# Kernel optimization log

Measured on AMD Instinct MI355X. Metric: run time of the kernel, lower is better.

## Reference

```python
import jax, jax.numpy as jnp
import numpy as np

H, D, DM, L, B = 16, 64, 1024, 256, 64
SCALE = 1.0 / np.sqrt(D)   # 1/sqrt(d_head)
CHUNK = 64
LN_EPS = 1e-5


def setup_inputs() -> dict:
    key = jax.random.key(0)
    k0, k1, k2, k3 = jax.random.split(key, 4)
    h = jax.random.normal(k0, (L, B, DM), jnp.float32)
    qkv_w = jax.random.normal(k1, (H * 4 * D, DM), jnp.float32) * 0.02
    o_w = jax.random.normal(k2, (DM, H * D), jnp.float32) * 0.02
    ln_gamma = jnp.ones((DM,), jnp.float32)
    ln_beta = jnp.zeros((DM,), jnp.float32)
    pi0 = jax.random.uniform(k3, (H, 256), jnp.float32)
    return {"h": h, "qkv_w": qkv_w, "o_w": o_w,
            "ln_gamma": ln_gamma, "ln_beta": ln_beta, "pi0": pi0}


def _phi(x):
    # elu(x) + 1, then sum-normalize over feature dim
    e = jax.nn.elu(x) + 1.0
    return e / e.sum(-1, keepdims=True)


def _fast_weight_sum(q, k, v):
    # q,k,v: [B,H,L,D]. out[t] = q_t @ W_t, W_t = sum_{s<=t} k_s v_s^T (inclusive).
    # Chunked-recurrent form: intra-chunk causal GEMM + inter-chunk carried state.
    Bb, Hh, Ll, Dd = q.shape
    nc = Ll // CHUNK
    rs = lambda x: x.reshape(Bb, Hh, nc, CHUNK, Dd).transpose(2, 0, 1, 3, 4)  # [nc,B,H,C,D]
    qc, kc, vc = rs(q), rs(k), rs(v)
    mask = jnp.tril(jnp.ones((CHUNK, CHUNK), q.dtype))  # inclusive causal

    def step(W, xs):
        qi, ki, vi = xs  # [B,H,C,D]
        scores = jnp.einsum('bhtd,bhsd->bhts', qi, ki) * mask
        out = jnp.einsum('bhts,bhsd->bhtd', scores, vi) \
            + jnp.einsum('bhtd,bhde->bhte', qi, W)
        W = W + jnp.einsum('bhsd,bhse->bhde', ki, vi)
        return W, out

    W0 = jnp.zeros((Bb, Hh, Dd, Dd), q.dtype)
    _, outs = jax.lax.scan(step, W0, (qc, kc, vc))  # outs: [nc,B,H,C,D]
    return outs.transpose(1, 2, 0, 3, 4).reshape(Bb, Hh, Ll, Dd)


def reference(h, qkv_w, o_w, ln_gamma, ln_beta, pi0):
    slen, bsz, _ = h.shape
    # qkv projection and head split (rbf2keys: q, k1, k2, v)
    qkv = (h @ qkv_w.T).reshape(slen, bsz, H, 4 * D)
    hq, hk1, hk2, hv = jnp.split(qkv, 4, axis=-1)       # each [L,B,H,D]
    perm = lambda x: x.transpose(1, 2, 0, 3)            # -> [B,H,L,D]
    hq, hk1, hk2, hv = perm(hq), perm(hk1), perm(hk2), perm(hv)

    hq = _phi(hq)
    hk1 = _phi(hk1)
    hk2 = _phi(hk2)

    out1 = _fast_weight_sum(hq, hk1, hv)
    out2 = _fast_weight_sum(hq, hk2, hv)

    # skip_attn_normalization=True path: pi0-gated mixture of the two memories
    p = jnp.clip(pi0, 0.0, 1.0)[None, :, :slen, None]   # [1,H,L,1]
    layer_out = SCALE * (out1 * p + out2 * (1.0 - p))   # [B,H,L,D]

    # [B,H,L,D] -> [L,B,H*D]
    layer_out = layer_out.transpose(0, 2, 1, 3).reshape(bsz, slen, H * D).transpose(1, 0, 2)
    attn_out = layer_out @ o_w.T                        # [L,B,DM]

    # post-LN residual (pre_lnorm=False)
    x = h + attn_out
    mu = x.mean(-1, keepdims=True)
    var = ((x - mu) ** 2).mean(-1, keepdims=True)
    return (x - mu) / jnp.sqrt(var + LN_EPS) * ln_gamma + ln_beta
```

## Files before the change

### kernel.cpp

```cpp
#include <hip/hip_runtime.h>
#include <type_traits>


typedef short v8s __attribute__((ext_vector_type(8)));
typedef float v4f __attribute__((ext_vector_type(4)));

__device__ __forceinline__ float bf2f(short s) {
    unsigned int u = ((unsigned int)(unsigned short)s) << 16;
    float f;
    __builtin_memcpy(&f, &u, 4);
    return f;
}
__device__ __forceinline__ short f2bf(float f) {
    unsigned int u;
    __builtin_memcpy(&u, &f, 4);
    u = u + 0x7fffu + ((u >> 16) & 1u);
    return (short)(u >> 16);
}

__device__ __forceinline__ void load_lds16(const short* g, short* l) {
    __builtin_amdgcn_global_load_lds((const __attribute__((address_space(1))) void*)g,
                                     (__attribute__((address_space(3))) void*)l, 16, 0, 0);
}

__global__ void __launch_bounds__(256)
cvt_bf16(const float* __restrict__ in, short* __restrict__ out, int n4) {
    int i = blockIdx.x * 256 + threadIdx.x;
    if (i >= n4) return;
    float4 v = ((const float4*)in)[i];
    short4 o;
    o.x = f2bf(v.x); o.y = f2bf(v.y); o.z = f2bf(v.z); o.w = f2bf(v.w);
    ((short4*)out)[i] = o;
}

template <typename OutT>
__global__ void __launch_bounds__(512, 2)
gemm_nt(const short* __restrict__ Ap, const short* __restrict__ Bp,
        OutT* __restrict__ C, int M, int N, int K) {
    __shared__ __align__(16) short lds[2][2][256 * 64];

    const int tid = threadIdx.x;
    const int w = tid >> 6, lane = tid & 63;
    const int wm = w >> 2, wn = w & 3;
    const int lq = lane >> 4, lr = lane & 15;
    const int asw = (lr & 7) * 8;
    const int rr = tid >> 3;
    const int scol = ((tid & 7) * 8) ^ ((rr & 7) * 8);

    int bid = blockIdx.y * gridDim.x + blockIdx.x;
    int nwg = gridDim.x * gridDim.y;
    int swz = (bid & 7) * (nwg >> 3) + (bid >> 3);
    int bm = swz % gridDim.x, bn = swz / gridDim.x;

    v4f acc[8][4] = {};
    v8s a[4][2];
    v8s b[2][2][2];

    const int NT = K >> 6;
    const int nIter = NT >> 1;

#define BAR_() do { asm volatile("" ::: "memory"); __builtin_amdgcn_s_barrier(); asm volatile("" ::: "memory"); } while (0)
#define SBAR_() __builtin_amdgcn_sched_barrier(0)
#define VMCNT4_() asm volatile("s_waitcnt vmcnt(4)" ::: "memory")
#define STAGE_(MAT, BUF, HALF, KT) do { \
        const short* g_ = ((MAT) ? Bp : Ap) + \
            (long)(((MAT) ? bn : bm) * 256 + (HALF) * 128 + rr) * K + (KT) * 64 + scol; \
        short* l_ = &lds[BUF][MAT][(HALF) * 8192] + w * 512; \
        load_lds16(g_, l_); \
        load_lds16(g_ + (long)64 * K, l_ + 4096); \
    } while (0)
#define LDA_(QM, BUF) do { \
        _Pragma("unroll") \
        for (int mi = 0; mi < 4; ++mi) { \
            const short* pa_ = &lds[BUF][0][(wm * 128 + (QM) * 64 + mi * 16 + lr) * 64]; \
            a[mi][0] = *(const v8s*)&pa_[(lq * 8) ^ asw]; \
            a[mi][1] = *(const v8s*)&pa_[(32 + lq * 8) ^ asw]; \
        } \
    } while (0)
#define LDB_(QN, BUF) do { \
        _Pragma("unroll") \
        for (int ni = 0; ni < 2; ++ni) { \
            const short* pb_ = &lds[BUF][1][(wn * 64 + (QN) * 32 + ni * 16 + lr) * 64]; \
            b[QN][ni][0] = *(const v8s*)&pb_[(lq * 8) ^ asw]; \
            b[QN][ni][1] = *(const v8s*)&pb_[(32 + lq * 8) ^ asw]; \
        } \
    } while (0)
#define MFMA_(QM, QN) do { \
        __builtin_amdgcn_s_setprio(1); \
        _Pragma("unroll") \
        for (int kk = 0; kk < 2; ++kk) \
            _Pragma("unroll") \
            for (int mi = 0; mi < 4; ++mi) \
                _Pragma("unroll") \
                for (int ni = 0; ni < 2; ++ni) \
                    acc[(QM) * 4 + mi][(QN) * 2 + ni] = __builtin_amdgcn_mfma_f32_16x16x32_bf16( \
                        a[mi][kk], b[QN][ni][kk], acc[(QM) * 4 + mi][(QN) * 2 + ni], 0, 0, 0); \
        __builtin_amdgcn_s_setprio(0); \
    } while (0)

    STAGE_(1, 0, 0, 0);
    STAGE_(1, 0, 1, 0);
    STAGE_(0, 0, 0, 0);
    STAGE_(0, 0, 1, 0);
    STAGE_(1, 1, 0, 1);
    STAGE_(1, 1, 1, 1);
    VMCNT4_();
    BAR_();

    for (int it = 0; it < nIter; ++it) {
        const int t1 = 2 * it + 1;
        int t2 = 2 * it + 2; if (t2 >= NT) t2 -= NT;
        int t3 = 2 * it + 3; if (t3 >= NT) t3 -= NT;

        LDA_(0, 0); LDB_(0, 0); LDB_(1, 0);
        STAGE_(0, 1, 0, t1);
        MFMA_(0, 0);
        SBAR_(); BAR_();
        STAGE_(0, 1, 1, t1);
        MFMA_(0, 1);
        SBAR_();
        LDA_(1, 0);
        SBAR_(); BAR_();
        STAGE_(1, 0, 0, t2);
        MFMA_(1, 0);
        SBAR_(); BAR_();
        STAGE_(1, 0, 1, t2);
        VMCNT4_();
        MFMA_(1, 1);
        SBAR_(); BAR_();
        LDA_(0, 1); LDB_(0, 1); LDB_(1, 1);
        STAGE_(0, 0, 0, t2);
        MFMA_(0, 0);
        SBAR_(); BAR_();
        STAGE_(0, 0, 1, t2);
        MFMA_(0, 1);
        SBAR_();
        LDA_(1, 1);
        SBAR_(); BAR_();
        STAGE_(1, 1, 0, t3);
        MFMA_(1, 0);
        SBAR_(); BAR_();
        STAGE_(1, 1, 1, t3);
        VMCNT4_();
        MFMA_(1, 1);
        SBAR_(); BAR_();
    }

#undef BAR_
#undef SBAR_
#undef VMCNT4_
#undef STAGE_
#undef LDA_
#undef LDB_
#undef MFMA_

#pragma unroll
    for (int m = 0; m < 8; ++m)
#pragma unroll
        for (int n = 0; n < 4; ++n)
#pragma unroll
            for (int r = 0; r < 4; ++r) {
                int row = bm * 256 + wm * 128 + m * 16 + lq * 4 + r;
                int col = bn * 256 + wn * 64 + n * 16 + lr;
                float v = acc[m][n][r];
                if constexpr (std::is_same_v<OutT, short>)
                    C[(long)row * N + col] = f2bf(v);
                else
                    C[(long)row * N + col] = v;
            }
}

#define SW(row, s) ((row) * 72 + ((((s) >> 3) ^ (((row) >> 4) & 7)) << 3) + ((s) & 7))

__device__ __forceinline__ void phi_store(const short* __restrict__ g,
                                          short* sS, short* sT, int r, int seg) {
    union { int4 v[2]; short s[16]; } u;
    u.v[0] = *(const int4*)(g);
    u.v[1] = *(const int4*)(g + 8);
    float f[16]; float ssum = 0.f;
#pragma unroll
    for (int i = 0; i < 16; i++) {
        float x = bf2f(u.s[i]);
        float e = x > 0.f ? x + 1.f : __expf(x);
        f[i] = e; ssum += e;
    }
    ssum += __shfl_xor(ssum, 1, 64);
    ssum += __shfl_xor(ssum, 2, 64);
    float inv = 1.f / ssum;
    union { int4 v[2]; short s[16]; } o;
#pragma unroll
    for (int i = 0; i < 16; i++) o.s[i] = f2bf(f[i] * inv);
    *(int4*)&sS[SW(r, seg)] = o.v[0];
    *(int4*)&sS[SW(r, seg + 8)] = o.v[1];
    if (sT) {
#pragma unroll
        for (int i = 0; i < 16; i++) sT[SW(seg + i, r)] = o.s[i];
    }
}

__global__ void __launch_bounds__(256)
fastweight(const short* __restrict__ qkv, const float* __restrict__ pi0,
           short* __restrict__ outm) {
    const int bid = blockIdx.x;
    const int h = bid & 15, b = bid >> 4;
    const int tid = threadIdx.x;
    const int w = tid >> 6, lane = tid & 63;
    const int lq = lane >> 4, lr = lane & 15;
    __shared__ __align__(16) short sq[64 * 72];
    __shared__ __align__(16) short sk1S[64 * 72];
    __shared__ __align__(16) short sk2S[64 * 72];
    __shared__ __align__(16) short sk1T[64 * 72];
    __shared__ __align__(16) short sk2T[64 * 72];
    __shared__ __align__(16) short svT[64 * 72];
    __shared__ __align__(16) short sW1T[64 * 72];
    __shared__ __align__(16) short sW2T[64 * 72];
    __shared__ float spi[256];

    for (int i = tid; i < 64 * 36; i += 256) { ((int*)sW1T)[i] = 0; ((int*)sW2T)[i] = 0; }
    spi[tid] = pi0[h * 256 + tid];

    const int r = tid >> 2, seg = (tid & 3) * 16;

    v4f wacc1[4] = {}, wacc2[4] = {};

    for (int c = 0; c < 4; c++) {
        __syncthreads();
        const long gbase = ((long)((c * 64 + r) * 64 + b)) * 4096 + h * 256;
        phi_store(qkv + gbase + seg, sq, nullptr, r, seg);
        phi_store(qkv + gbase + 64 + seg, sk1S, sk1T, r, seg);
        phi_store(qkv + gbase + 128 + seg, sk2S, sk2T, r, seg);
        {
            union { int4 v[2]; short s[16]; } u;
            u.v[0] = *(const int4*)(qkv + gbase + 192 + seg);
            u.v[1] = *(const int4*)(qkv + gbase + 192 + seg + 8);
#pragma unroll
            for (int i = 0; i < 16; i++) svT[SW(seg + i, r)] = u.s[i];
        }
        __syncthreads();

        v8s qa0 = *(const v8s*)&sq[SW(16 * w + lr, lq * 8)];
        v8s qa1 = *(const v8s*)&sq[SW(16 * w + lr, 32 + lq * 8)];

        v4f sacc1[4], sacc2[4];
#pragma unroll
        for (int n = 0; n < 4; n++) {
            v8s b10 = *(const v8s*)&sk1S[SW(16 * n + lr, lq * 8)];
            v8s b11 = *(const v8s*)&sk1S[SW(16 * n + lr, 32 + lq * 8)];
            v8s b20 = *(const v8s*)&sk2S[SW(16 * n + lr, lq * 8)];
            v8s b21 = *(const v8s*)&sk2S[SW(16 * n + lr, 32 + lq * 8)];
            v4f t1 = {}, t2 = {};
            t1 = __builtin_amdgcn_mfma_f32_16x16x32_bf16(qa0, b10, t1, 0, 0, 0);
            t2 = __builtin_amdgcn_mfma_f32_16x16x32_bf16(qa0, b20, t2, 0, 0, 0);
            t1 = __builtin_amdgcn_mfma_f32_16x16x32_bf16(qa1, b11, t1, 0, 0, 0);
            t2 = __builtin_amdgcn_mfma_f32_16x16x32_bf16(qa1, b21, t2, 0, 0, 0);
            sacc1[n] = t1; sacc2[n] = t2;
        }
        __syncthreads();
#pragma unroll
        for (int n = 0; n < 4; n++)
#pragma unroll
            for (int rr = 0; rr < 4; rr++) {
                int t_ = 16 * w + lq * 4 + rr;
                int s_ = 16 * n + lr;
                sk1S[SW(t_, s_)] = f2bf(s_ <= t_ ? sacc1[n][rr] : 0.f);
                sk2S[SW(t_, s_)] = f2bf(s_ <= t_ ? sacc2[n][rr] : 0.f);
            }

        v8s sa10 = *(const v8s*)&sk1S[SW(16 * w + lr, lq * 8)];
        v8s sa11 = *(const v8s*)&sk1S[SW(16 * w + lr, 32 + lq * 8)];
        v8s sa20 = *(const v8s*)&sk2S[SW(16 * w + lr, lq * 8)];
        v8s sa21 = *(const v8s*)&sk2S[SW(16 * w + lr, 32 + lq * 8)];
        v4f o1[4], o2[4];
#pragma unroll
        for (int n = 0; n < 4; n++) {
            v8s vb0 = *(const v8s*)&svT[SW(16 * n + lr, lq * 8)];
            v8s vb1 = *(const v8s*)&svT[SW(16 * n + lr, 32 + lq * 8)];
            v8s wb10 = *(const v8s*)&sW1T[SW(16 * n + lr, lq * 8)];
            v8s wb11 = *(const v8s*)&sW1T[SW(16 * n + lr, 32 + lq * 8)];
            v8s wb20 = *(const v8s*)&sW2T[SW(16 * n + lr, lq * 8)];
            v8s wb21 = *(const v8s*)&sW2T[SW(16 * n + lr, 32 + lq * 8)];
            v4f t1 = {}, t2 = {};
            t1 = __builtin_amdgcn_mfma_f32_16x16x32_bf16(sa10, vb0, t1, 0, 0, 0);
            t2 = __builtin_amdgcn_mfma_f32_16x16x32_bf16(sa20, vb0, t2, 0, 0, 0);
            t1 = __builtin_amdgcn_mfma_f32_16x16x32_bf16(sa11, vb1, t1, 0, 0, 0);
            t2 = __builtin_amdgcn_mfma_f32_16x16x32_bf16(sa21, vb1, t2, 0, 0, 0);
            t1 = __builtin_amdgcn_mfma_f32_16x16x32_bf16(qa0, wb10, t1, 0, 0, 0);
            t2 = __builtin_amdgcn_mfma_f32_16x16x32_bf16(qa0, wb20, t2, 0, 0, 0);
            t1 = __builtin_amdgcn_mfma_f32_16x16x32_bf16(qa1, wb11, t1, 0, 0, 0);
            t2 = __builtin_amdgcn_mfma_f32_16x16x32_bf16(qa1, wb21, t2, 0, 0, 0);
            o1[n] = t1; o2[n] = t2;
        }
#pragma unroll
        for (int n = 0; n < 4; n++)
#pragma unroll
            for (int rr = 0; rr < 4; rr++) {
                int t_ = 16 * w + lq * 4 + rr;
                int l = c * 64 + t_;
                float p = fminf(fmaxf(spi[l], 0.f), 1.f);
                float val = 0.125f * (p * o1[n][rr] + (1.f - p) * o2[n][rr]);
                long o = ((long)(l * 64 + b)) * 1024 + h * 64 + 16 * n + lr;
                outm[o] = f2bf(val);
            }

        if (c < 3) {
            __syncthreads();
            v8s va0 = *(const v8s*)&svT[SW(16 * w + lr, lq * 8)];
            v8s va1 = *(const v8s*)&svT[SW(16 * w + lr, 32 + lq * 8)];
#pragma unroll
            for (int n = 0; n < 4; n++) {
                v8s kb10 = *(const v8s*)&sk1T[SW(16 * n + lr, lq * 8)];
                v8s kb11 = *(const v8s*)&sk1T[SW(16 * n + lr, 32 + lq * 8)];
                v8s kb20 = *(const v8s*)&sk2T[SW(16 * n + lr, lq * 8)];
                v8s kb21 = *(const v8s*)&sk2T[SW(16 * n + lr, 32 + lq * 8)];
                wacc1[n] = __builtin_amdgcn_mfma_f32_16x16x32_bf16(va0, kb10, wacc1[n], 0, 0, 0);
                wacc2[n] = __builtin_amdgcn_mfma_f32_16x16x32_bf16(va0, kb20, wacc2[n], 0, 0, 0);
                wacc1[n] = __builtin_amdgcn_mfma_f32_16x16x32_bf16(va1, kb11, wacc1[n], 0, 0, 0);
                wacc2[n] = __builtin_amdgcn_mfma_f32_16x16x32_bf16(va1, kb21, wacc2[n], 0, 0, 0);
            }
#pragma unroll
            for (int n = 0; n < 4; n++)
#pragma unroll
                for (int rr = 0; rr < 4; rr++) {
                    sW1T[SW(16 * w + lq * 4 + rr, 16 * n + lr)] = f2bf(wacc1[n][rr]);
                    sW2T[SW(16 * w + lq * 4 + rr, 16 * n + lr)] = f2bf(wacc2[n][rr]);
                }
        }
    }
}

__global__ void __launch_bounds__(256)
ln_kernel(const float* __restrict__ h, const float* __restrict__ attn,
          const float* __restrict__ gamma, const float* __restrict__ beta,
          float* __restrict__ out) {
    const int row = blockIdx.x;
    const long base = (long)row * 1024;
    const int tid = threadIdx.x;
    float4 xh = ((const float4*)(h + base))[tid];
    float4 xa = ((const float4*)(attn + base))[tid];
    float4 x;
    x.x = xh.x + xa.x; x.y = xh.y + xa.y; x.z = xh.z + xa.z; x.w = xh.w + xa.w;
    float s = x.x + x.y + x.z + x.w;
    float s2 = x.x * x.x + x.y * x.y + x.z * x.z + x.w * x.w;
#pragma unroll
    for (int m = 32; m > 0; m >>= 1) {
        s += __shfl_xor(s, m, 64);
        s2 += __shfl_xor(s2, m, 64);
    }
    __shared__ float ps[4], ps2[4];
    int w = tid >> 6, lane = tid & 63;
    if (lane == 0) { ps[w] = s; ps2[w] = s2; }
    __syncthreads();
    s = ps[0] + ps[1] + ps[2] + ps[3];
    s2 = ps2[0] + ps2[1] + ps2[2] + ps2[3];
    float mu = s * (1.f / 1024.f);
    float var = s2 * (1.f / 1024.f) - mu * mu;
    float inv = rsqrtf(var + 1e-5f);
    float4 g = ((const float4*)gamma)[tid];
    float4 bb = ((const float4*)beta)[tid];
    float4 o;
    o.x = (x.x - mu) * inv * g.x + bb.x;
    o.y = (x.y - mu) * inv * g.y + bb.y;
    o.z = (x.z - mu) * inv * g.z + bb.z;
    o.w = (x.w - mu) * inv * g.w + bb.w;
    ((float4*)(out + base))[tid] = o;
}

extern "C" void kernel_launch(void* const* d_in, const int* in_sizes, int n_in,
                              void* d_out, int out_size, void* d_ws, size_t ws_size,
                              hipStream_t stream) {
    const float* h     = (const float*)d_in[0];
    const float* qkvw  = (const float*)d_in[1];
    const float* ow    = (const float*)d_in[2];
    const float* gamma = (const float*)d_in[3];
    const float* beta  = (const float*)d_in[4];
    const float* pi0   = (const float*)d_in[5];
    float* out = (float*)d_out;
    char* ws = (char*)d_ws;

    short* h_bf   = (short*)(ws);
    short* wq_bf  = (short*)(ws + 33554432);
    short* wo_bf  = (short*)(ws + 41943040);
    short* qkv_bf = (short*)(ws + 44040192);
    float* attnf  = (float*)(ws + 44040192);
    short* lmix   = h_bf;

    cvt_bf16<<<16384, 256, 0, stream>>>(h, h_bf, 16777216 / 4);
    cvt_bf16<<<4096, 256, 0, stream>>>(qkvw, wq_bf, 4194304 / 4);
    cvt_bf16<<<1024, 256, 0, stream>>>(ow, wo_bf, 1048576 / 4);

    gemm_nt<short><<<dim3(64, 16), 512, 0, stream>>>(h_bf, wq_bf, qkv_bf, 16384, 4096, 1024);

    fastweight<<<1024, 256, 0, stream>>>(qkv_bf, pi0, lmix);

    gemm_nt<float><<<dim3(64, 4), 512, 0, stream>>>(lmix, wo_bf, attnf, 16384, 1024, 1024);

    ln_kernel<<<16384, 256, 0, stream>>>(h, attnf, gamma, beta, out);
}
```

Baseline: 419.4 us.

## Prefetch next chunk in fastweight, repack LDS swizzle, remap GEMM tiles

The fastweight kernel now loads the next chunk's q/k1/k2/v from global memory into registers before processing the current chunk, so load latency overlaps the MFMA work. The LDS tiles drop their padding and use an XOR swizzle, which shrinks shared memory so two blocks can fit per CU (launch bounds 256,2). The GEMM also gets a new tile mapping for gridDim.x==64 that groups M tiles per XCD for L2 locality. The cost is higher register pressure from the prefetch buffers, which could cause spills under the tighter launch bound.

Result: faster. 405.8 us (-3.3%).

```diff
diff --git a/kernel.cpp b/kernel.cpp
--- a/kernel.cpp
+++ b/kernel.cpp
@@ -48,9 +48,16 @@
     const int scol = ((tid & 7) * 8) ^ ((rr & 7) * 8);
 
     int bid = blockIdx.y * gridDim.x + blockIdx.x;
-    int nwg = gridDim.x * gridDim.y;
-    int swz = (bid & 7) * (nwg >> 3) + (bid >> 3);
-    int bm = swz % gridDim.x, bn = swz / gridDim.x;
+    int bm, bn;
+    if (gridDim.x == 64) {
+        int xcd = bid & 7, u = bid >> 3;
+        bm = xcd * 8 + (u & 7);
+        bn = u >> 3;
+    } else {
+        int nwg = gridDim.x * gridDim.y;
+        int swz = (bid & 7) * (nwg >> 3) + (bid >> 3);
+        bm = swz % gridDim.x; bn = swz / gridDim.x;
+    }
 
     v4f acc[8][4] = {};
     v8s a[4][2];
@@ -170,13 +177,12 @@
             }
 }
 
-#define SW(row, s) ((row) * 72 + ((((s) >> 3) ^ (((row) >> 4) & 7)) << 3) + ((s) & 7))
-
-__device__ __forceinline__ void phi_store(const short* __restrict__ g,
-                                          short* sS, short* sT, int r, int seg) {
-    union { int4 v[2]; short s[16]; } u;
-    u.v[0] = *(const int4*)(g);
-    u.v[1] = *(const int4*)(g + 8);
+#define SW(row, s) (((row) << 6) + ((s) ^ (((((row) >> 4) ^ (row)) & 7) << 3)))
+
+union FW16 { int4 v[2]; short s[16]; };
+
+__device__ __forceinline__ void phi_to_lds(const FW16& u, short* sS, short* sT,
+                                           int r, int seg) {
     float f[16]; float ssum = 0.f;
 #pragma unroll
     for (int i = 0; i < 16; i++) {
@@ -187,7 +193,7 @@
     ssum += __shfl_xor(ssum, 1, 64);
     ssum += __shfl_xor(ssum, 2, 64);
     float inv = 1.f / ssum;
-    union { int4 v[2]; short s[16]; } o;
+    FW16 o;
 #pragma unroll
     for (int i = 0; i < 16; i++) o.s[i] = f2bf(f[i] * inv);
     *(int4*)&sS[SW(r, seg)] = o.v[0];
@@ -198,7 +204,7 @@
     }
 }
 
-__global__ void __launch_bounds__(256)
+__global__ void __launch_bounds__(256, 2)
 fastweight(const short* __restrict__ qkv, const float* __restrict__ pi0,
            short* __restrict__ outm) {
     const int bid = blockIdx.x;
@@ -206,36 +212,48 @@
     const int tid = threadIdx.x;
     const int w = tid >> 6, lane = tid & 63;
     const int lq = lane >> 4, lr = lane & 15;
-    __shared__ __align__(16) short sq[64 * 72];
-    __shared__ __align__(16) short sk1S[64 * 72];
-    __shared__ __align__(16) short sk2S[64 * 72];
-    __shared__ __align__(16) short sk1T[64 * 72];
-    __shared__ __align__(16) short sk2T[64 * 72];
-    __shared__ __align__(16) short svT[64 * 72];
-    __shared__ __align__(16) short sW1T[64 * 72];
-    __shared__ __align__(16) short sW2T[64 * 72];
+    __shared__ __align__(16) short sq[64 * 64];
+    __shared__ __align__(16) short sk1S[64 * 64];
+    __shared__ __align__(16) short sk2S[64 * 64];
+    __shared__ __align__(16) short sk1T[64 * 64];
+    __shared__ __align__(16) short sk2T[64 * 64];
+    __shared__ __align__(16) short svT[64 * 64];
+    __shared__ __align__(16) short sW1T[64 * 64];
+    __shared__ __align__(16) short sW2T[64 * 64];
     __shared__ float spi[256];
 
-    for (int i = tid; i < 64 * 36; i += 256) { ((int*)sW1T)[i] = 0; ((int*)sW2T)[i] = 0; }
+    for (int i = tid; i < 2048; i += 256) { ((int*)sW1T)[i] = 0; ((int*)sW2T)[i] = 0; }
     spi[tid] = pi0[h * 256 + tid];
 
     const int r = tid >> 2, seg = (tid & 3) * 16;
 
     v4f wacc1[4] = {}, wacc2[4] = {};
 
+    FW16 cq, ck1, ck2, cv;
+    {
+        const short* g = qkv + ((long)(r * 64 + b)) * 4096 + h * 256 + seg;
+        cq.v[0]  = *(const int4*)(g);        cq.v[1]  = *(const int4*)(g + 8);
+        ck1.v[0] = *(const int4*)(g + 64);   ck1.v[1] = *(const int4*)(g + 72);
+        ck2.v[0] = *(const int4*)(g + 128);  ck2.v[1] = *(const int4*)(g + 136);
+        cv.v[0]  = *(const int4*)(g + 192);  cv.v[1]  = *(const int4*)(g + 200);
+    }
+
+#pragma unroll
     for (int c = 0; c < 4; c++) {
+        FW16 nq, nk1, nk2, nv;
+        if (c < 3) {
+            const short* g = qkv + ((long)(((c + 1) * 64 + r) * 64 + b)) * 4096 + h * 256 + seg;
+            nq.v[0]  = *(const int4*)(g);        nq.v[1]  = *(const int4*)(g + 8);
+            nk1.v[0] = *(const int4*)(g + 64);   nk1.v[1] = *(const int4*)(g + 72);
+            nk2.v[0] = *(const int4*)(g + 128);  nk2.v[1] = *(const int4*)(g + 136);
+            nv.v[0]  = *(const int4*)(g + 192);  nv.v[1]  = *(const int4*)(g + 200);
+        }
         __syncthreads();
-        const long gbase = ((long)((c * 64 + r) * 64 + b)) * 4096 + h * 256;
-        phi_store(qkv + gbase + seg, sq, nullptr, r, seg);
-        phi_store(qkv + gbase + 64 + seg, sk1S, sk1T, r, seg);
-        phi_store(qkv + gbase + 128 + seg, sk2S, sk2T, r, seg);
-        {
-            union { int4 v[2]; short s[16]; } u;
-            u.v[0] = *(const int4*)(qkv + gbase + 192 + seg);
-            u.v[1] = *(const int4*)(qkv + gbase + 192 + seg + 8);
-#pragma unroll
-            for (int i = 0; i < 16; i++) svT[SW(seg + i, r)] = u.s[i];
-        }
+        phi_to_lds(cq, sq, nullptr, r, seg);
+        phi_to_lds(ck1, sk1S, sk1T, r, seg);
+        phi_to_lds(ck2, sk2S, sk2T, r, seg);
+#pragma unroll
+        for (int i = 0; i < 16; i++) svT[SW(seg + i, r)] = cv.s[i];
         __syncthreads();
 
         v8s qa0 = *(const v8s*)&sq[SW(16 * w + lr, lq * 8)];
@@ -325,6 +343,7 @@
                     sW2T[SW(16 * w + lq * 4 + rr, 16 * n + lr)] = f2bf(wacc2[n][rr]);
                 }
         }
+        cq = nq; ck1 = nk1; ck2 = nk2; cv = nv;
     }
 }
 
```
